# Kernel tuning notes

Hardware: AMD Instinct MI355X
Metric: run time of the kernel (lower is better)

Reference implementation:

```python
import jax, jax.numpy as jnp
import numpy as np

I, H, O = 32, 64, 8  # input_size, hidden_layer, output_size
B, T = 4096, 256


def setup_inputs() -> dict:
    key = jax.random.key(0)
    ks = jax.random.split(key, 7)
    s_ih = 1.0 / np.sqrt(H)
    return {
        "x": jax.random.normal(ks[0], (B, T, I), dtype=jnp.float32),
        # PyTorch nn.LSTM params, gate order [i, f, g, o]
        "W_ih": jax.random.uniform(ks[1], (4 * H, I), jnp.float32, -s_ih, s_ih),
        "W_hh": jax.random.uniform(ks[2], (4 * H, H), jnp.float32, -s_ih, s_ih),
        "b_ih": jax.random.uniform(ks[3], (4 * H,), jnp.float32, -s_ih, s_ih),
        "b_hh": jax.random.uniform(ks[4], (4 * H,), jnp.float32, -s_ih, s_ih),
        "W_fc": jax.random.uniform(ks[5], (O, H), jnp.float32, -s_ih, s_ih),
        "b_fc": jax.random.uniform(ks[6], (O,), jnp.float32, -s_ih, s_ih),
    }


def reference(x, W_ih, W_hh, b_ih, b_hh, W_fc, b_fc):
    # Precompute input-to-hidden projections for all timesteps in one GEMM.
    # [B, T, 4H]
    x_proj = jnp.einsum('bti,gi->btg', x, W_ih) + b_ih + b_hh

    def step(carry, xp_t):
        h, c = carry  # [B, H] each
        gates = xp_t + h @ W_hh.T  # [B, 4H]
        i_g, f_g, g_g, o_g = jnp.split(gates, 4, axis=-1)
        i_g = jax.nn.sigmoid(i_g)
        f_g = jax.nn.sigmoid(f_g)
        g_g = jnp.tanh(g_g)
        o_g = jax.nn.sigmoid(o_g)
        c = f_g * c + i_g * g_g
        h = o_g * jnp.tanh(c)
        return (h, c), None

    h0 = jnp.zeros((x.shape[0], H), dtype=x.dtype)
    c0 = jnp.zeros((x.shape[0], H), dtype=x.dtype)
    # scan over time axis: move T to leading axis
    (h_T, c_T), _ = jax.lax.scan(step, (h0, c0), jnp.swapaxes(x_proj, 0, 1))
    # out[:, -1, :] == final hidden state for single-layer batch_first LSTM
    return h_T @ W_fc.T + b_fc
```

## Files before the change

### kernel.cpp

```cpp
#include <hip/hip_runtime.h>
#include <hip/hip_bf16.h>


#define T_LEN 256
#define I_SZ  32
#define H_SZ  64
#define O_SZ  8
#define BR    16

typedef __attribute__((ext_vector_type(8))) short short8;
typedef __attribute__((ext_vector_type(4))) float f32x4;

static __device__ __forceinline__ short f2bf(float f) {
    union { __hip_bfloat16 b; short s; } u;
    u.b = __float2bfloat16(f);
    return u.s;
}

static __device__ __forceinline__ float rcp_fast(float x) {
    return __builtin_amdgcn_rcpf(x);
}
static __device__ __forceinline__ float sigf(float x) {
    return rcp_fast(1.0f + __expf(-x));
}
static __device__ __forceinline__ float tanh_fast(float x) {
    return 1.0f - 2.0f * rcp_fast(1.0f + __expf(2.0f * x));
}

__global__ __launch_bounds__(256, 1)
void lstm_fused_kernel(const float* __restrict__ x,
                       const float* __restrict__ W_ih,
                       const float* __restrict__ W_hh,
                       const float* __restrict__ b_ih,
                       const float* __restrict__ b_hh,
                       const float* __restrict__ W_fc,
                       const float* __restrict__ b_fc,
                       float* __restrict__ out)
{
    __shared__ short A_lds[16][104];
    __shared__ float Hf[16][64];

    const int tid  = threadIdx.x;
    const int wave = tid >> 6;
    const int lane = tid & 63;
    const int quad = lane >> 4;
    const int nlow = lane & 15;
    const int j    = wave * 16 + nlow;
    const int b0   = blockIdx.x * BR;

    short8 bfrag[4][3];
    for (int g = 0; g < 4; ++g) {
        const int col = g * 64 + j;
        {
            const float* wr = W_ih + col * I_SZ + quad * 8;
            short8 f;
            #pragma unroll
            for (int e = 0; e < 8; ++e) f[e] = f2bf(wr[e]);
            bfrag[g][0] = f;
        }
        #pragma unroll
        for (int kt = 1; kt < 3; ++kt) {
            const float* wr = W_hh + col * H_SZ + (kt - 1) * 32 + quad * 8;
            short8 f;
            #pragma unroll
            for (int e = 0; e < 8; ++e) f[e] = f2bf(wr[e]);
            bfrag[g][kt] = f;
        }
    }
    float bias[4];
    #pragma unroll
    for (int g = 0; g < 4; ++g) bias[g] = b_ih[g * 64 + j] + b_hh[g * 64 + j];

    for (int q = tid; q < 16 * 64; q += 256)
        A_lds[q >> 6][32 + (q & 63)] = (short)0;

    float c[4]  = {0.f, 0.f, 0.f, 0.f};
    float hq[4] = {0.f, 0.f, 0.f, 0.f};

    const int xr = tid >> 4;
    const int xi = (tid & 15) * 2;
    const float* xbase = x + ((size_t)(b0 + xr) * T_LEN) * I_SZ + xi;
    float2 xreg = *(const float2*)(xbase);

    for (int t = 0; t < T_LEN; ++t) {
        A_lds[xr][xi]     = f2bf(xreg.x);
        A_lds[xr][xi + 1] = f2bf(xreg.y);
        __syncthreads();

        if (t + 1 < T_LEN) xreg = *(const float2*)(xbase + (t + 1) * I_SZ);

        short8 a0 = *(const short8*)&A_lds[nlow][0 * 32 + quad * 8];
        short8 a1 = *(const short8*)&A_lds[nlow][1 * 32 + quad * 8];
        short8 a2 = *(const short8*)&A_lds[nlow][2 * 32 + quad * 8];

        f32x4 acc[4];
        #pragma unroll
        for (int g = 0; g < 4; ++g) {
            f32x4 a = {0.f, 0.f, 0.f, 0.f};
            a = __builtin_amdgcn_mfma_f32_16x16x32_bf16(a0, bfrag[g][0], a, 0, 0, 0);
            a = __builtin_amdgcn_mfma_f32_16x16x32_bf16(a1, bfrag[g][1], a, 0, 0, 0);
            a = __builtin_amdgcn_mfma_f32_16x16x32_bf16(a2, bfrag[g][2], a, 0, 0, 0);
            acc[g] = a;
        }
        __syncthreads();

        #pragma unroll
        for (int q = 0; q < 4; ++q) {
            float iv = sigf(acc[0][q] + bias[0]);
            float fv = sigf(acc[1][q] + bias[1]);
            float gv = tanh_fast(acc[2][q] + bias[2]);
            float ov = sigf(acc[3][q] + bias[3]);
            c[q] = fv * c[q] + iv * gv;
            float hv = ov * tanh_fast(c[q]);
            hq[q] = hv;
            A_lds[quad * 4 + q][32 + j] = f2bf(hv);
        }
    }

    #pragma unroll
    for (int q = 0; q < 4; ++q) Hf[quad * 4 + q][j] = hq[q];
    __syncthreads();

    if (tid < BR * O_SZ) {
        const int r = tid >> 3;
        const int o = tid & 7;
        const float* wf = W_fc + o * H_SZ;
        float acc = b_fc[o];
        #pragma unroll
        for (int jx = 0; jx < H_SZ; ++jx) acc += Hf[r][jx] * wf[jx];
        out[(size_t)(b0 + r) * O_SZ + o] = acc;
    }
}

extern "C" void kernel_launch(void* const* d_in, const int* in_sizes, int n_in,
                              void* d_out, int out_size, void* d_ws, size_t ws_size,
                              hipStream_t stream) {
    const float* x    = (const float*)d_in[0];
    const float* W_ih = (const float*)d_in[1];
    const float* W_hh = (const float*)d_in[2];
    const float* b_ih = (const float*)d_in[3];
    const float* b_hh = (const float*)d_in[4];
    const float* W_fc = (const float*)d_in[5];
    const float* b_fc = (const float*)d_in[6];
    float* out = (float*)d_out;

    const int B = 4096;
    lstm_fused_kernel<<<dim3(B / BR), dim3(256), 0, stream>>>(
        x, W_ih, W_hh, b_ih, b_hh, W_fc, b_fc, out);
}
```

Before: 327.0 us.

## Halve rows per block and redistribute gate activations through LDS

Each block now handles 8 batch rows instead of 16, so twice as many blocks launch and launch bounds allow two blocks per CU. The MFMA tiles still compute 16 rows, with the upper 8 padded with zeros. The accumulators for the valid rows are written to a new shared buffer, and every thread then computes the nonlinearities for two (row, hidden) pairs. This spreads the elementwise gate work over more threads per row and raises occupancy. The cost is an extra LDS round trip per timestep, half of the MFMA work spent on padding, and more blocks each reloading the weights.

After: 324.8 us. Within noise of the previous version (-0.7%).

```diff
diff --git a/kernel.cpp b/kernel.cpp
--- a/kernel.cpp
+++ b/kernel.cpp
@@ -6,7 +6,7 @@
 #define I_SZ  32
 #define H_SZ  64
 #define O_SZ  8
-#define BR    16
+#define BR    8
 
 typedef __attribute__((ext_vector_type(8))) short short8;
 typedef __attribute__((ext_vector_type(4))) float f32x4;
@@ -27,7 +27,7 @@
     return 1.0f - 2.0f * rcp_fast(1.0f + __expf(2.0f * x));
 }
 
-__global__ __launch_bounds__(256, 1)
+__global__ __launch_bounds__(256, 2)
 void lstm_fused_kernel(const float* __restrict__ x,
                        const float* __restrict__ W_ih,
                        const float* __restrict__ W_hh,
@@ -38,19 +38,20 @@
                        float* __restrict__ out)
 {
     __shared__ short A_lds[16][104];
-    __shared__ float Hf[16][64];
+    __shared__ float G[4][BR][64];
+    __shared__ float Hf[BR][64];
 
     const int tid  = threadIdx.x;
     const int wave = tid >> 6;
     const int lane = tid & 63;
     const int quad = lane >> 4;
     const int nlow = lane & 15;
-    const int j    = wave * 16 + nlow;
+    const int jw   = wave * 16 + nlow;
     const int b0   = blockIdx.x * BR;
 
     short8 bfrag[4][3];
     for (int g = 0; g < 4; ++g) {
-        const int col = g * 64 + j;
+        const int col = g * 64 + jw;
         {
             const float* wr = W_ih + col * I_SZ + quad * 8;
             short8 f;
@@ -67,27 +68,27 @@
             bfrag[g][kt] = f;
         }
     }
+
+    const int jr = tid & 63;
+    const int r0 = tid >> 6;
+    const int r1 = r0 + 4;
     float bias[4];
     #pragma unroll
-    for (int g = 0; g < 4; ++g) bias[g] = b_ih[g * 64 + j] + b_hh[g * 64 + j];
+    for (int g = 0; g < 4; ++g) bias[g] = b_ih[g * 64 + jr] + b_hh[g * 64 + jr];
 
-    for (int q = tid; q < 16 * 64; q += 256)
-        A_lds[q >> 6][32 + (q & 63)] = (short)0;
+    const int xr = tid >> 5;
+    const int xi = tid & 31;
+    const float* xbase = x + ((size_t)(b0 + xr) * T_LEN) * I_SZ + xi;
+    float xreg = xbase[0];
 
-    float c[4]  = {0.f, 0.f, 0.f, 0.f};
-    float hq[4] = {0.f, 0.f, 0.f, 0.f};
+    for (int q = tid; q < 16 * 104; q += 256) ((short*)A_lds)[q] = (short)0;
 
-    const int xr = tid >> 4;
-    const int xi = (tid & 15) * 2;
-    const float* xbase = x + ((size_t)(b0 + xr) * T_LEN) * I_SZ + xi;
-    float2 xreg = *(const float2*)(xbase);
+    float c0 = 0.f, c1 = 0.f, hv0 = 0.f, hv1 = 0.f;
 
     for (int t = 0; t < T_LEN; ++t) {
-        A_lds[xr][xi]     = f2bf(xreg.x);
-        A_lds[xr][xi + 1] = f2bf(xreg.y);
+        A_lds[xr][xi] = f2bf(xreg);
         __syncthreads();
-
-        if (t + 1 < T_LEN) xreg = *(const float2*)(xbase + (t + 1) * I_SZ);
+        if (t + 1 < T_LEN) xreg = xbase[(t + 1) * I_SZ];
 
         short8 a0 = *(const short8*)&A_lds[nlow][0 * 32 + quad * 8];
         short8 a1 = *(const short8*)&A_lds[nlow][1 * 32 + quad * 8];
@@ -102,23 +103,40 @@
             a = __builtin_amdgcn_mfma_f32_16x16x32_bf16(a2, bfrag[g][2], a, 0, 0, 0);
             acc[g] = a;
         }
+        if (quad < 2) {
+            #pragma unroll
+            for (int g = 0; g < 4; ++g) {
+                #pragma unroll
+                for (int q = 0; q < 4; ++q)
+                    G[g][quad * 4 + q][jw] = acc[g][q];
+            }
+        }
         __syncthreads();
 
+        float p0[4], p1[4];
         #pragma unroll
-        for (int q = 0; q < 4; ++q) {
-            float iv = sigf(acc[0][q] + bias[0]);
-            float fv = sigf(acc[1][q] + bias[1]);
-            float gv = tanh_fast(acc[2][q] + bias[2]);
-            float ov = sigf(acc[3][q] + bias[3]);
-            c[q] = fv * c[q] + iv * gv;
-            float hv = ov * tanh_fast(c[q]);
-            hq[q] = hv;
-            A_lds[quad * 4 + q][32 + j] = f2bf(hv);
+        for (int g = 0; g < 4; ++g) {
+            p0[g] = G[g][r0][jr] + bias[g];
+            p1[g] = G[g][r1][jr] + bias[g];
+        }
+        {
+            float iv = sigf(p0[0]), fv = sigf(p0[1]);
+            float gv = tanh_fast(p0[2]), ov = sigf(p0[3]);
+            c0 = fv * c0 + iv * gv;
+            hv0 = ov * tanh_fast(c0);
+            A_lds[r0][32 + jr] = f2bf(hv0);
+        }
+        {
+            float iv = sigf(p1[0]), fv = sigf(p1[1]);
+            float gv = tanh_fast(p1[2]), ov = sigf(p1[3]);
+            c1 = fv * c1 + iv * gv;
+            hv1 = ov * tanh_fast(c1);
+            A_lds[r1][32 + jr] = f2bf(hv1);
         }
     }
 
-    #pragma unroll
-    for (int q = 0; q < 4; ++q) Hf[quad * 4 + q][j] = hq[q];
+    Hf[r0][jr] = hv0;
+    Hf[r1][jr] = hv1;
     __syncthreads();
 
     if (tid < BR * O_SZ) {
```

## Halve batch rows per block, double-buffer hidden state, load x directly into registers

Applied to the files above, without the earlier changes.

Each block now handles 8 batch rows instead of 16, which doubles the grid and allows two blocks per CU. The hidden state is double-buffered in LDS, so each step needs one barrier instead of two. The x operand now goes from global memory straight into MFMA fragments with a two-step prefetch, and the bias is folded into the MFMA accumulator init. In exchange, half of each 16-row MFMA tile is wasted: the padded rows are computed but their gate math is skipped.

Result: slower. 466.8 us (+42.7%).

```diff
diff --git a/kernel.cpp b/kernel.cpp
--- a/kernel.cpp
+++ b/kernel.cpp
@@ -6,7 +6,8 @@
 #define I_SZ  32
 #define H_SZ  64
 #define O_SZ  8
-#define BR    16
+#define BR    8
+#define HS    72
 
 typedef __attribute__((ext_vector_type(8))) short short8;
 typedef __attribute__((ext_vector_type(4))) float f32x4;
@@ -16,18 +17,19 @@
     u.b = __float2bfloat16(f);
     return u.s;
 }
-
-static __device__ __forceinline__ float rcp_fast(float x) {
-    return __builtin_amdgcn_rcpf(x);
-}
 static __device__ __forceinline__ float sigf(float x) {
-    return rcp_fast(1.0f + __expf(-x));
+    return __builtin_amdgcn_rcpf(1.0f + __expf(-x));
 }
 static __device__ __forceinline__ float tanh_fast(float x) {
-    return 1.0f - 2.0f * rcp_fast(1.0f + __expf(2.0f * x));
+    return 1.0f - 2.0f * __builtin_amdgcn_rcpf(1.0f + __expf(2.0f * x));
 }
 
-__global__ __launch_bounds__(256, 1)
+#define BAR() do { \
+    asm volatile("s_waitcnt lgkmcnt(0)" ::: "memory"); \
+    __builtin_amdgcn_s_barrier(); \
+} while (0)
+
+__global__ __launch_bounds__(256, 2)
 void lstm_fused_kernel(const float* __restrict__ x,
                        const float* __restrict__ W_ih,
                        const float* __restrict__ W_hh,
@@ -37,20 +39,23 @@
                        const float* __restrict__ b_fc,
                        float* __restrict__ out)
 {
-    __shared__ short A_lds[16][104];
-    __shared__ float Hf[16][64];
+    __shared__ short hbuf[2][16][HS];
+    __shared__ float Hf[BR][64];
 
     const int tid  = threadIdx.x;
     const int wave = tid >> 6;
     const int lane = tid & 63;
     const int quad = lane >> 4;
     const int nlow = lane & 15;
-    const int j    = wave * 16 + nlow;
+    const int jw   = wave * 16 + nlow;
     const int b0   = blockIdx.x * BR;
 
+    for (int q = tid; q < 2 * 16 * HS; q += 256) ((short*)hbuf)[q] = (short)0;
+
     short8 bfrag[4][3];
+    float  biasg[4];
     for (int g = 0; g < 4; ++g) {
-        const int col = g * 64 + j;
+        const int col = g * 64 + jw;
         {
             const float* wr = W_ih + col * I_SZ + quad * 8;
             short8 f;
@@ -66,60 +71,67 @@
             for (int e = 0; e < 8; ++e) f[e] = f2bf(wr[e]);
             bfrag[g][kt] = f;
         }
+        biasg[g] = b_ih[col] + b_hh[col];
     }
-    float bias[4];
-    #pragma unroll
-    for (int g = 0; g < 4; ++g) bias[g] = b_ih[g * 64 + j] + b_hh[g * 64 + j];
 
-    for (int q = tid; q < 16 * 64; q += 256)
-        A_lds[q >> 6][32 + (q & 63)] = (short)0;
+    const int xrow = min(b0 + nlow, 4096 - 1);
+    const float* xb = x + ((size_t)xrow * T_LEN) * I_SZ + quad * 8;
+
+    float4 pa = *(const float4*)(xb + 0);
+    float4 pb = *(const float4*)(xb + 4);
+    float4 qa = *(const float4*)(xb + I_SZ);
+    float4 qb = *(const float4*)(xb + I_SZ + 4);
 
     float c[4]  = {0.f, 0.f, 0.f, 0.f};
-    float hq[4] = {0.f, 0.f, 0.f, 0.f};
-
-    const int xr = tid >> 4;
-    const int xi = (tid & 15) * 2;
-    const float* xbase = x + ((size_t)(b0 + xr) * T_LEN) * I_SZ + xi;
-    float2 xreg = *(const float2*)(xbase);
+    float hv[4] = {0.f, 0.f, 0.f, 0.f};
 
     for (int t = 0; t < T_LEN; ++t) {
-        A_lds[xr][xi]     = f2bf(xreg.x);
-        A_lds[xr][xi + 1] = f2bf(xreg.y);
-        __syncthreads();
+        short8 ax;
+        ax[0] = f2bf(pa.x); ax[1] = f2bf(pa.y);
+        ax[2] = f2bf(pa.z); ax[3] = f2bf(pa.w);
+        ax[4] = f2bf(pb.x); ax[5] = f2bf(pb.y);
+        ax[6] = f2bf(pb.z); ax[7] = f2bf(pb.w);
+        pa = qa; pb = qb;
+        if (t + 2 < T_LEN) {
+            qa = *(const float4*)(xb + (t + 2) * I_SZ);
+            qb = *(const float4*)(xb + (t + 2) * I_SZ + 4);
+        }
 
-        if (t + 1 < T_LEN) xreg = *(const float2*)(xbase + (t + 1) * I_SZ);
+        BAR();
 
-        short8 a0 = *(const short8*)&A_lds[nlow][0 * 32 + quad * 8];
-        short8 a1 = *(const short8*)&A_lds[nlow][1 * 32 + quad * 8];
-        short8 a2 = *(const short8*)&A_lds[nlow][2 * 32 + quad * 8];
+        const short* hrow = &hbuf[t & 1][nlow][quad * 8];
+        short8 a1 = *(const short8*)(hrow);
+        short8 a2 = *(const short8*)(hrow + 32);
 
         f32x4 acc[4];
         #pragma unroll
         for (int g = 0; g < 4; ++g) {
-            f32x4 a = {0.f, 0.f, 0.f, 0.f};
-            a = __builtin_amdgcn_mfma_f32_16x16x32_bf16(a0, bfrag[g][0], a, 0, 0, 0);
+            f32x4 a = {biasg[g], biasg[g], biasg[g], biasg[g]};
+            a = __builtin_amdgcn_mfma_f32_16x16x32_bf16(ax, bfrag[g][0], a, 0, 0, 0);
             a = __builtin_amdgcn_mfma_f32_16x16x32_bf16(a1, bfrag[g][1], a, 0, 0, 0);
             a = __builtin_amdgcn_mfma_f32_16x16x32_bf16(a2, bfrag[g][2], a, 0, 0, 0);
             acc[g] = a;
         }
-        __syncthreads();
 
-        #pragma unroll
-        for (int q = 0; q < 4; ++q) {
-            float iv = sigf(acc[0][q] + bias[0]);
-            float fv = sigf(acc[1][q] + bias[1]);
-            float gv = tanh_fast(acc[2][q] + bias[2]);
-            float ov = sigf(acc[3][q] + bias[3]);
-            c[q] = fv * c[q] + iv * gv;
-            float hv = ov * tanh_fast(c[q]);
-            hq[q] = hv;
-            A_lds[quad * 4 + q][32 + j] = f2bf(hv);
+        if (quad < 2) {
+            #pragma unroll
+            for (int q = 0; q < 4; ++q) {
+                float iv = sigf(acc[0][q]);
+                float fv = sigf(acc[1][q]);
+                float gv = tanh_fast(acc[2][q]);
+                float ov = sigf(acc[3][q]);
+                c[q] = fv * c[q] + iv * gv;
+                hv[q] = ov * tanh_fast(c[q]);
+                hbuf[(t + 1) & 1][quad * 4 + q][jw] = f2bf(hv[q]);
+            }
         }
     }
 
-    #pragma unroll
-    for (int q = 0; q < 4; ++q) Hf[quad * 4 + q][j] = hq[q];
-    __syncthreads();
+    if (quad < 2) {
+        #pragma unroll
+        for (int q = 0; q < 4; ++q) Hf[quad * 4 + q][jw] = hv[q];
+    }
+    BAR();
 
     if (tid < BR * O_SZ) {
         const int r = tid >> 3;
```
